# Performance work log

Hardware: AMD Instinct MI355X
Metric: run time of the kernel (lower is better)

## Reference

```python
import jax, jax.numpy as jnp
import numpy as np

EPS_SCALE = 1e-4

def setup_inputs() -> dict:
    key = jax.random.key(0)
    B, D, K = 4096, 64, 256
    x = jax.random.normal(key, (B, D, K), dtype=jnp.float32)
    return {"x": x}

def reference(x):
    # x: [B, D, K]  (batch, cluster_dim, num_clusters) -- training path
    B, D, K = x.shape
    mu = jnp.mean(x, axis=0, keepdims=True)              # [1, D, K]
    xc = jnp.transpose(x - mu, (2, 1, 0))                # [K, D, B]
    cov = jnp.einsum('kdb,keb->kde', xc, xc) / (B - 1)   # [K, D, D]
    eps = EPS_SCALE * jnp.eye(D, dtype=x.dtype)
    L = jnp.linalg.cholesky(cov + eps)                   # [K, D, D]
    Z = jax.scipy.linalg.solve_triangular(L, xc, lower=True)  # [K, D, B]
    return jnp.transpose(Z, (2, 1, 0))                   # [B, D, K]
```

## Files before the change

### kernel.cpp

```cpp
#include <hip/hip_runtime.h>
#include <math.h>

#define Bn 4096
#define Dn 64
#define Kn 256
#define DKn 16384
#define SLAB ((size_t)262144)

typedef __attribute__((ext_vector_type(8))) short bf16x8;
typedef __attribute__((ext_vector_type(4))) float f32x4;
typedef unsigned short u16;
typedef unsigned int u32;

__device__ __forceinline__ float bf2f(u16 u) {
  return __uint_as_float(((u32)u) << 16);
}
__device__ __forceinline__ u16 f2bf(float f) {
  u32 x = __float_as_uint(f);
  u32 r = x + 0x7fffu + ((x >> 16) & 1u);
  return (u16)(r >> 16);
}

__global__ __launch_bounds__(256) void k1_transpose(
    const float* __restrict__ x, u16* __restrict__ xh) {
  __shared__ float tf[64][65];
  const int b0 = blockIdx.x * 8;
  const int k0 = blockIdx.y * 64;
  const int t = threadIdx.x;
  const int kq = t & 15, dsub = t >> 4;
  const int dq = t & 7, kr = t >> 3;

  for (int bb = 0; bb < 8; ++bb) {
    const int b = b0 + bb;
#pragma unroll
    for (int i = 0; i < 4; ++i) {
      const int d = dsub + 16 * i;
      const float4 v = *(const float4*)&x[(size_t)b * DKn + (size_t)d * Kn + k0 + 4 * kq];
      tf[4 * kq + 0][d] = v.x;
      tf[4 * kq + 1][d] = v.y;
      tf[4 * kq + 2][d] = v.z;
      tf[4 * kq + 3][d] = v.w;
    }
    __syncthreads();
#pragma unroll
    for (int it = 0; it < 2; ++it) {
      const int k = kr + 32 * it;
      u32 pk[4];
#pragma unroll
      for (int j = 0; j < 4; ++j) {
        const float f0 = tf[k][8 * dq + 2 * j];
        const float f1 = tf[k][8 * dq + 2 * j + 1];
        pk[j] = (u32)f2bf(f0) | ((u32)f2bf(f1) << 16);
      }
      *(uint4*)&xh[(size_t)(k0 + k) * SLAB + (size_t)b * 64 + 8 * dq] =
          make_uint4(pk[0], pk[1], pk[2], pk[3]);
    }
    __syncthreads();
  }
}

__global__ __launch_bounds__(256) void k2_cov(
    const u16* __restrict__ xh, float* __restrict__ covp, float* __restrict__ Sp) {
  __shared__ __align__(16) u16 tile[64][136];
  __shared__ float sred[64][33];
  const int part = blockIdx.x;
  const int k = blockIdx.y;
  const int t = threadIdx.x;
  const int w = t >> 6, l = t & 63;
  const int r16 = l & 15, g = l >> 4;
  const int q = t >> 3, c = t & 7;
  const u16* pk = xh + (size_t)k * SLAB;

  f32x4 hh[10];
#pragma unroll
  for (int p = 0; p < 10; ++p) hh[p] = (f32x4){0.f, 0.f, 0.f, 0.f};
  float dsums[8];
#pragma unroll
  for (int jj = 0; jj < 8; ++jj) dsums[jj] = 0.f;

  for (int sub = 0; sub < 8; ++sub) {
    const int bbase = part * 1024 + sub * 128;
    __syncthreads();
    uint4 pv[4];
#pragma unroll
    for (int i = 0; i < 4; ++i)
      pv[i] = *(const uint4*)&pk[(size_t)(bbase + 4 * q + i) * 64 + c * 8];
    const u16* e0 = (const u16*)&pv[0];
    const u16* e1 = (const u16*)&pv[1];
    const u16* e2 = (const u16*)&pv[2];
    const u16* e3 = (const u16*)&pv[3];
#pragma unroll
    for (int jj = 0; jj < 8; ++jj) {
      const int d = 8 * c + jj;
      const int s4 = 4 * ((d >> 2) & 7);
      const u16 v0 = e0[jj], v1 = e1[jj], v2 = e2[jj], v3 = e3[jj];
      dsums[jj] += (bf2f(v0) + bf2f(v1)) + (bf2f(v2) + bf2f(v3));
      const int col0 = (2 * q) ^ s4;
      uint2 st;
      st.x = (u32)v0 | ((u32)v1 << 16);
      st.y = (u32)v2 | ((u32)v3 << 16);
      *(uint2*)&tile[d][2 * col0] = st;
    }
    __syncthreads();
    bf16x8 fr[4];
#pragma unroll
    for (int m = 0; m < 4; ++m) {
      const int d = 16 * m + r16;
      const int s4 = 4 * ((d >> 2) & 7);
      const int colb = (16 * w + 4 * g) ^ s4;
      fr[m] = *(const bf16x8*)&tile[d][2 * colb];
    }
#pragma unroll
    for (int m = 0; m < 4; ++m)
#pragma unroll
      for (int n = m; n < 4; ++n) {
        const int p = (m * (7 - m)) / 2 + n;
        hh[p] = __builtin_amdgcn_mfma_f32_16x16x32_bf16(fr[m], fr[n], hh[p], 0, 0, 0);
      }
  }
  float* cp = covp + ((size_t)k * 16 + part * 4 + w) * 2560;
#pragma unroll
  for (int p = 0; p < 10; ++p)
#pragma unroll
    for (int r = 0; r < 4; ++r)
      cp[p * 256 + (g * 4 + r) * 16 + r16] = hh[p][r];
#pragma unroll
  for (int jj = 0; jj < 8; ++jj) sred[8 * c + jj][q] = dsums[jj];
  __syncthreads();
  if (t < 64) {
    float s = 0.f;
#pragma unroll
    for (int q2 = 0; q2 < 32; ++q2) s += sred[t][q2];
    Sp[((size_t)k * 4 + part) * 64 + t] = s;
  }
}

__global__ __launch_bounds__(256) void k3_chol(
    const float* __restrict__ covp, const float* __restrict__ Sp,
    u16* __restrict__ wt, u16* __restrict__ vout) {
  __shared__ float a[64][65];
  __shared__ float mus[64];
  __shared__ float colv[64];
  __shared__ float diag;
  const int k = blockIdx.x;
  const int tid = threadIdx.x;
  if (tid < 64) {
    float s = 0.f;
#pragma unroll
    for (int q = 0; q < 4; ++q) s += Sp[((size_t)k * 4 + q) * 64 + tid];
    mus[tid] = s * (1.f / 4096.f);
  }
  __syncthreads();
  const float* cp = covp + (size_t)k * 16 * 2560;
  for (int idx = tid; idx < 4096; idx += 256) {
    const int i = idx >> 6, j = idx & 63;
    const int i16 = i >> 4, j16 = j >> 4, r = i & 15, c = j & 15;
    int p, off;
    if (i16 <= j16) { p = (i16 * (7 - i16)) / 2 + j16; off = r * 16 + c; }
    else            { p = (j16 * (7 - j16)) / 2 + i16; off = c * 16 + r; }
    float s = 0.f;
#pragma unroll
    for (int q = 0; q < 16; ++q) s += cp[q * 2560 + p * 256 + off];
    float cv = (s - 4096.f * mus[i] * mus[j]) * (1.f / 4095.f);
    if (i == j) cv += 1e-4f;
    a[i][j] = cv;
  }
  __syncthreads();
  for (int j = 0; j < 64; ++j) {
    if (tid == j) diag = sqrtf(a[j][j]);
    __syncthreads();
    const float ljj = diag;
    float lij = 0.f;
    if (tid == j) a[j][j] = ljj;
    if (tid < 64 && tid > j) {
      lij = a[tid][j] / ljj;
      a[tid][j] = lij;
      colv[tid] = lij;
    }
    __syncthreads();
    if (tid < 64 && tid > j)
      for (int e = j + 1; e <= tid; ++e) a[tid][e] -= lij * colv[e];
    __syncthreads();
  }
  float wv[64];
  if (tid < 64) {
#pragma unroll
    for (int i = 0; i < 64; ++i) {
      float s2 = (i == tid) ? 1.f : 0.f;
#pragma unroll
      for (int j = 0; j < i; ++j) s2 -= a[i][j] * wv[j];
      wv[i] = (i >= tid) ? s2 / a[i][i] : 0.f;
    }
  }
  __syncthreads();
  if (tid < 64) {
#pragma unroll
    for (int i = 0; i < 64; ++i) a[i][tid] = wv[i];
  }
  __syncthreads();
  if (tid < 64) {
    float v = 0.f;
#pragma unroll
    for (int e = 0; e < 64; ++e) v += a[tid][e] * mus[e];
    vout[(size_t)k * 64 + tid] = f2bf(v);
  }
#pragma unroll
  for (int it = 0; it < 8; ++it) {
    const int idx = it * 256 + tid;
    const int dd = idx >> 5, ep = idx & 31;
    const u32 pk2 = (u32)f2bf(a[dd][2 * ep]) | ((u32)f2bf(a[dd][2 * ep + 1]) << 16);
    *(u32*)&wt[(size_t)k * 4096 + 2 * idx] = pk2;
  }
}

union __align__(16) SMemU {
  u16 xstage[2][8][16][64];
  u32 zls[16 * 642 + 40];
};

__global__ __launch_bounds__(256) void k45_solve(
    const u16* __restrict__ xh, const u16* __restrict__ wt,
    const u16* __restrict__ vin, float* __restrict__ out) {
  __shared__ SMemU sm;
  __shared__ __align__(16) u16 vsh[32][72];
  const int b0 = blockIdx.x * 16;
  const int kc0 = blockIdx.y * 32;
  const int t = threadIdx.x;
  const int w = t >> 6, l = t & 63;
  const int r16 = l & 15, g = l >> 4;
  const int d0 = 16 * w + 4 * g;

  *(uint4*)&vsh[t >> 3][8 * (t & 7)] = *(const uint4*)&vin[(size_t)kc0 * 64 + t * 8];

  uint4 sv[4];
#pragma unroll
  for (int i = 0; i < 4; ++i) {
    const int idx = i * 256 + t;
    const int kk = idx >> 7, b = (idx >> 3) & 15, dc = idx & 7;
    sv[i] = *(const uint4*)&xh[(size_t)(kc0 + kk) * SLAB + (size_t)(b0 + b) * 64 + dc * 8];
  }
#pragma unroll
  for (int i = 0; i < 4; ++i) {
    const int idx = i * 256 + t;
    const int kk = idx >> 7, b = (idx >> 3) & 15, dc = idx & 7;
    *(uint4*)&sm.xstage[0][kk][b][(dc ^ (b & 7)) * 8] = sv[i];
  }

  bf16x8 af0[4], af1[4];
#pragma unroll
  for (int p = 0; p < 4; ++p) {
    const u16* wk = wt + (size_t)(kc0 + p) * 4096 + (16 * w + r16) * 64 + 8 * g;
    af0[p] = *(const bf16x8*)(wk);
    af1[p] = *(const bf16x8*)(wk + 32);
  }
  __syncthreads();

  u32 zr[64];

#pragma unroll
  for (int rnd = 0; rnd < 4; ++rnd) {
    if (rnd < 3) {
#pragma unroll
      for (int i = 0; i < 4; ++i) {
        const int idx = i * 256 + t;
        const int kk = idx >> 7, b = (idx >> 3) & 15, dc = idx & 7;
        sv[i] = *(const uint4*)&xh[(size_t)(kc0 + (rnd + 1) * 8 + kk) * SLAB +
                                   (size_t)(b0 + b) * 64 + dc * 8];
      }
    }
#pragma unroll
    for (int kk = 0; kk < 8; ++kk) {
      const int kidx = rnd * 8 + kk;
      const bf16x8 a0 = af0[kidx & 3];
      const bf16x8 a1 = af1[kidx & 3];
      if (kidx + 4 < 32) {
        const u16* wk = wt + (size_t)(kc0 + kidx + 4) * 4096 + (16 * w + r16) * 64 + 8 * g;
        af0[kidx & 3] = *(const bf16x8*)(wk);
        af1[kidx & 3] = *(const bf16x8*)(wk + 32);
      }
      const bf16x8 bf0 = *(const bf16x8*)&sm.xstage[rnd & 1][kk][r16][(g ^ (r16 & 7)) * 8];
      const bf16x8 bf1 = *(const bf16x8*)&sm.xstage[rnd & 1][kk][r16][((4 + g) ^ (r16 & 7)) * 8];
      f32x4 acc = (f32x4){0.f, 0.f, 0.f, 0.f};
      acc = __builtin_amdgcn_mfma_f32_16x16x32_bf16(a0, bf0, acc, 0, 0, 0);
      acc = __builtin_amdgcn_mfma_f32_16x16x32_bf16(a1, bf1, acc, 0, 0, 0);
      const uint2 vv = *(const uint2*)&vsh[kidx][d0];
      const float s0 = acc[0] - __uint_as_float(vv.x << 16);
      const float s1 = acc[1] - __uint_as_float(vv.x & 0xffff0000u);
      const float s2 = acc[2] - __uint_as_float(vv.y << 16);
      const float s3 = acc[3] - __uint_as_float(vv.y & 0xffff0000u);
      u32 plo, phi;
      asm("v_cvt_pk_bf16_f32 %0, %1, %2" : "=v"(plo) : "v"(s0), "v"(s1));
      asm("v_cvt_pk_bf16_f32 %0, %1, %2" : "=v"(phi) : "v"(s2), "v"(s3));
      zr[2 * kidx] = plo;
      zr[2 * kidx + 1] = phi;
    }
    if (rnd < 3) {
#pragma unroll
      for (int i = 0; i < 4; ++i) {
        const int idx = i * 256 + t;
        const int kk = idx >> 7, b = (idx >> 3) & 15, dc = idx & 7;
        *(uint4*)&sm.xstage[(rnd + 1) & 1][kk][b][(dc ^ (b & 7)) * 8] = sv[i];
      }
      __syncthreads();
    }
  }
  __syncthreads();

#pragma unroll
  for (int h = 0; h < 2; ++h) {
    u32 W[4][8];
#pragma unroll
    for (int r = 0; r < 4; ++r)
#pragma unroll
      for (int q2 = 0; q2 < 8; ++q2) {
        const int k2 = 16 * h + 2 * q2;
        const u32 za = zr[2 * k2 + (r >> 1)];
        const u32 zb2 = zr[2 * (k2 + 1) + (r >> 1)];
        W[r][q2] = (r & 1) ? ((za >> 16) | (zb2 & 0xffff0000u))
                           : ((za & 0xffffu) | (zb2 << 16));
      }
#pragma unroll
    for (int r = 0; r < 4; ++r) {
      u32* cp = &sm.zls[r16 * 642 + (d0 + r) * 10];
      *(uint2*)&cp[0] = make_uint2(W[r][0], W[r][1]);
      *(uint2*)&cp[2] = make_uint2(W[r][2], W[r][3]);
      *(uint2*)&cp[4] = make_uint2(W[r][4], W[r][5]);
      *(uint2*)&cp[6] = make_uint2(W[r][6], W[r][7]);
    }
    __syncthreads();
#pragma unroll
    for (int it = 0; it < 16; ++it) {
      const int c = w * 256 + it * 16 + (l >> 2);
      const int kc = l & 3;
      const int b = c >> 6, d = c & 63;
      const uint2 zw = *(const uint2*)&sm.zls[b * 642 + d * 10 + 2 * kc];
      float4 ov;
      ov.x = __uint_as_float(zw.x << 16);
      ov.y = __uint_as_float(zw.x & 0xffff0000u);
      ov.z = __uint_as_float(zw.y << 16);
      ov.w = __uint_as_float(zw.y & 0xffff0000u);
      *(float4*)&out[(size_t)(b0 + b) * DKn + (size_t)d * Kn + kc0 + 16 * h + 4 * kc] = ov;
    }
    __syncthreads();
  }
}

extern "C" void kernel_launch(void* const* d_in, const int* in_sizes, int n_in,
                              void* d_out, int out_size, void* d_ws, size_t ws_size,
                              hipStream_t stream) {
  (void)in_sizes; (void)n_in; (void)out_size;
  const float* x = (const float*)d_in[0];
  float* out = (float*)d_out;
  char* ws = (char*)d_ws;
  const size_t XH_B = 134217728;
  const size_t CP_B = 41943040;
  const size_t SP_B = 262144;
  const size_t WT_B = 2097152;
  const size_t V_B  = 32768;
  if (ws_size < XH_B + CP_B + SP_B + WT_B + V_B) return;
  u16* xh = (u16*)ws;
  float* covp = (float*)(ws + XH_B);
  float* Sp = (float*)(ws + XH_B + CP_B);
  u16* wtb = (u16*)(ws + XH_B + CP_B + SP_B);
  u16* vb  = (u16*)(ws + XH_B + CP_B + SP_B + WT_B);

  k1_transpose<<<dim3(512, 4), 256, 0, stream>>>(x, xh);
  k2_cov<<<dim3(4, 256), 256, 0, stream>>>(xh, covp, Sp);
  k3_chol<<<dim3(256), 256, 0, stream>>>(covp, Sp, wtb, vb);
  k45_solve<<<dim3(256, 8), 256, 0, stream>>>(xh, wtb, vb, out);
}
```

Measured before the change: 361.6 us.

## Double-buffer LDS in transpose and covariance kernels; single-wave Cholesky without barriers

The transpose and covariance kernels now double-buffer their shared-memory tiles. The next slab's global loads are issued before the current tile is consumed, and each iteration needs only one barrier instead of two. The Cholesky kernel runs the factorisation, inversion and mean projection in a single 64-lane wavefront, using LDS waitcnt fences instead of block-wide __syncthreads. This costs more LDS and registers in exchange for load overlap, and relies on wavefront-synchronous execution being correct.

New measurement: 357.5 us. Within noise of the previous version (-1.2%).

```diff
diff --git a/kernel.cpp b/kernel.cpp
--- a/kernel.cpp
+++ b/kernel.cpp
@@ -20,49 +20,77 @@
   u32 r = x + 0x7fffu + ((x >> 16) & 1u);
   return (u16)(r >> 16);
 }
+__device__ __forceinline__ void wave_lds_fence() {
+  asm volatile("s_waitcnt lgkmcnt(0)" ::: "memory");
+  __builtin_amdgcn_sched_barrier(0);
+}
 
 __global__ __launch_bounds__(256) void k1_transpose(
     const float* __restrict__ x, u16* __restrict__ xh) {
-  __shared__ float tf[64][65];
+  __shared__ float tf[2][64][65];
   const int b0 = blockIdx.x * 8;
   const int k0 = blockIdx.y * 64;
   const int t = threadIdx.x;
   const int kq = t & 15, dsub = t >> 4;
   const int dq = t & 7, kr = t >> 3;
 
+  float4 rv[4];
+#pragma unroll
+  for (int i = 0; i < 4; ++i)
+    rv[i] = *(const float4*)&x[(size_t)b0 * DKn + (size_t)(dsub + 16 * i) * Kn + k0 + 4 * kq];
+#pragma unroll
+  for (int i = 0; i < 4; ++i) {
+    const int d = dsub + 16 * i;
+    tf[0][4 * kq + 0][d] = rv[i].x;
+    tf[0][4 * kq + 1][d] = rv[i].y;
+    tf[0][4 * kq + 2][d] = rv[i].z;
+    tf[0][4 * kq + 3][d] = rv[i].w;
+  }
+  __syncthreads();
+
   for (int bb = 0; bb < 8; ++bb) {
-    const int b = b0 + bb;
-#pragma unroll
-    for (int i = 0; i < 4; ++i) {
-      const int d = dsub + 16 * i;
-      const float4 v = *(const float4*)&x[(size_t)b * DKn + (size_t)d * Kn + k0 + 4 * kq];
-      tf[4 * kq + 0][d] = v.x;
-      tf[4 * kq + 1][d] = v.y;
-      tf[4 * kq + 2][d] = v.z;
-      tf[4 * kq + 3][d] = v.w;
-    }
-    __syncthreads();
+    const int cur = bb & 1;
+    if (bb < 7) {
+#pragma unroll
+      for (int i = 0; i < 4; ++i)
+        rv[i] = *(const float4*)&x[(size_t)(b0 + bb + 1) * DKn +
+                                   (size_t)(dsub + 16 * i) * Kn + k0 + 4 * kq];
+    }
 #pragma unroll
     for (int it = 0; it < 2; ++it) {
       const int k = kr + 32 * it;
       u32 pk[4];
 #pragma unroll
       for (int j = 0; j < 4; ++j) {
-        const float f0 = tf[k][8 * dq + 2 * j];
-        const float f1 = tf[k][8 * dq + 2 * j + 1];
+        const float f0 = tf[cur][k][8 * dq + 2 * j];
+        const float f1 = tf[cur][k][8 * dq + 2 * j + 1];
         pk[j] = (u32)f2bf(f0) | ((u32)f2bf(f1) << 16);
       }
-      *(uint4*)&xh[(size_t)(k0 + k) * SLAB + (size_t)b * 64 + 8 * dq] =
+      *(uint4*)&xh[(size_t)(k0 + k) * SLAB + (size_t)(b0 + bb) * 64 + 8 * dq] =
           make_uint4(pk[0], pk[1], pk[2], pk[3]);
     }
-    __syncthreads();
-  }
-}
+    if (bb < 7) {
+#pragma unroll
+      for (int i = 0; i < 4; ++i) {
+        const int d = dsub + 16 * i;
+        tf[cur ^ 1][4 * kq + 0][d] = rv[i].x;
+        tf[cur ^ 1][4 * kq + 1][d] = rv[i].y;
+        tf[cur ^ 1][4 * kq + 2][d] = rv[i].z;
+        tf[cur ^ 1][4 * kq + 3][d] = rv[i].w;
+      }
+      __syncthreads();
+    }
+  }
+}
+
+union __align__(16) K2SMem {
+  u16 tile[2][64][136];
+  float sred[64][33];
+};
 
 __global__ __launch_bounds__(256) void k2_cov(
     const u16* __restrict__ xh, float* __restrict__ covp, float* __restrict__ Sp) {
-  __shared__ __align__(16) u16 tile[64][136];
-  __shared__ float sred[64][33];
+  __shared__ K2SMem s2;
   const int part = blockIdx.x;
   const int k = blockIdx.y;
   const int t = threadIdx.x;
@@ -78,37 +106,45 @@
 #pragma unroll
   for (int jj = 0; jj < 8; ++jj) dsums[jj] = 0.f;
 
+  uint4 pv[4];
+#define K2_LOAD(SUB)                                                           \
+  {                                                                            \
+    const int bbase = part * 1024 + (SUB) * 128;                               \
+    _Pragma("unroll") for (int i = 0; i < 4; ++i)                              \
+        pv[i] = *(const uint4*)&pk[(size_t)(bbase + 4 * q + i) * 64 + c * 8];  \
+  }
+#define K2_STORE(BUF)                                                          \
+  {                                                                            \
+    const u16* e0 = (const u16*)&pv[0];                                        \
+    const u16* e1 = (const u16*)&pv[1];                                        \
+    const u16* e2 = (const u16*)&pv[2];                                        \
+    const u16* e3 = (const u16*)&pv[3];                                        \
+    _Pragma("unroll") for (int jj = 0; jj < 8; ++jj) {                         \
+      const int d = 8 * c + jj;                                                \
+      const int s4 = 4 * ((d >> 2) & 7);                                       \
+      const u16 v0 = e0[jj], v1 = e1[jj], v2 = e2[jj], v3 = e3[jj];            \
+      dsums[jj] += (bf2f(v0) + bf2f(v1)) + (bf2f(v2) + bf2f(v3));              \
+      const int col0 = (2 * q) ^ s4;                                           \
+      uint2 st;                                                                \
+      st.x = (u32)v0 | ((u32)v1 << 16);                                        \
+      st.y = (u32)v2 | ((u32)v3 << 16);                                        \
+      *(uint2*)&s2.tile[BUF][d][2 * col0] = st;                                \
+    }                                                                          \
+  }
+
+  K2_LOAD(0);
+  K2_STORE(0);
+  __syncthreads();
   for (int sub = 0; sub < 8; ++sub) {
-    const int bbase = part * 1024 + sub * 128;
-    __syncthreads();
-    uint4 pv[4];
-#pragma unroll
-    for (int i = 0; i < 4; ++i)
-      pv[i] = *(const uint4*)&pk[(size_t)(bbase + 4 * q + i) * 64 + c * 8];
-    const u16* e0 = (const u16*)&pv[0];
-    const u16* e1 = (const u16*)&pv[1];
-    const u16* e2 = (const u16*)&pv[2];
-    const u16* e3 = (const u16*)&pv[3];
-#pragma unroll
-    for (int jj = 0; jj < 8; ++jj) {
-      const int d = 8 * c + jj;
-      const int s4 = 4 * ((d >> 2) & 7);
-      const u16 v0 = e0[jj], v1 = e1[jj], v2 = e2[jj], v3 = e3[jj];
-      dsums[jj] += (bf2f(v0) + bf2f(v1)) + (bf2f(v2) + bf2f(v3));
-      const int col0 = (2 * q) ^ s4;
-      uint2 st;
-      st.x = (u32)v0 | ((u32)v1 << 16);
-      st.y = (u32)v2 | ((u32)v3 << 16);
-      *(uint2*)&tile[d][2 * col0] = st;
-    }
-    __syncthreads();
+    const int cur = sub & 1;
+    if (sub < 7) K2_LOAD(sub + 1);
     bf16x8 fr[4];
 #pragma unroll
     for (int m = 0; m < 4; ++m) {
       const int d = 16 * m + r16;
       const int s4 = 4 * ((d >> 2) & 7);
       const int colb = (16 * w + 4 * g) ^ s4;
-      fr[m] = *(const bf16x8*)&tile[d][2 * colb];
+      fr[m] = *(const bf16x8*)&s2.tile[cur][d][2 * colb];
     }
 #pragma unroll
     for (int m = 0; m < 4; ++m)
@@ -117,6 +153,10 @@
         const int p = (m * (7 - m)) / 2 + n;
         hh[p] = __builtin_amdgcn_mfma_f32_16x16x32_bf16(fr[m], fr[n], hh[p], 0, 0, 0);
       }
+    if (sub < 7) {
+      K2_STORE(cur ^ 1);
+      __syncthreads();
+    }
   }
   float* cp = covp + ((size_t)k * 16 + part * 4 + w) * 2560;
 #pragma unroll
@@ -124,13 +164,14 @@
 #pragma unroll
     for (int r = 0; r < 4; ++r)
       cp[p * 256 + (g * 4 + r) * 16 + r16] = hh[p][r];
-#pragma unroll
-  for (int jj = 0; jj < 8; ++jj) sred[8 * c + jj][q] = dsums[jj];
+  __syncthreads();
+#pragma unroll
+  for (int jj = 0; jj < 8; ++jj) s2.sred[8 * c + jj][q] = dsums[jj];
   __syncthreads();
   if (t < 64) {
     float s = 0.f;
 #pragma unroll
-    for (int q2 = 0; q2 < 32; ++q2) s += sred[t][q2];
+    for (int q2 = 0; q2 < 32; ++q2) s += s2.sred[t][q2];
     Sp[((size_t)k * 4 + part) * 64 + t] = s;
   }
 }
@@ -141,7 +182,6 @@
   __shared__ float a[64][65];
   __shared__ float mus[64];
   __shared__ float colv[64];
-  __shared__ float diag;
   const int k = blockIdx.x;
   const int tid = threadIdx.x;
   if (tid < 64) {
@@ -166,24 +206,25 @@
     a[i][j] = cv;
   }
   __syncthreads();
-  for (int j = 0; j < 64; ++j) {
-    if (tid == j) diag = sqrtf(a[j][j]);
-    __syncthreads();
-    const float ljj = diag;
-    float lij = 0.f;
-    if (tid == j) a[j][j] = ljj;
-    if (tid < 64 && tid > j) {
-      lij = a[tid][j] / ljj;
-      a[tid][j] = lij;
-      colv[tid] = lij;
-    }
-    __syncthreads();
-    if (tid < 64 && tid > j)
-      for (int e = j + 1; e <= tid; ++e) a[tid][e] -= lij * colv[e];
-    __syncthreads();
-  }
-  float wv[64];
+
   if (tid < 64) {
+    for (int j = 0; j < 64; ++j) {
+      wave_lds_fence();
+      const float ljj = sqrtf(a[j][j]);
+      float lij = 0.f;
+      if (tid == j) a[j][j] = ljj;
+      if (tid > j) {
+        lij = a[tid][j] / ljj;
+        a[tid][j] = lij;
+        colv[tid] = lij;
+      }
+      wave_lds_fence();
+      if (tid > j) {
+        for (int e = j + 1; e <= tid; ++e) a[tid][e] -= lij * colv[e];
+      }
+    }
+    wave_lds_fence();
+    float wv[64];
 #pragma unroll
     for (int i = 0; i < 64; ++i) {
       float s2 = (i == tid) ? 1.f : 0.f;
@@ -191,19 +232,16 @@
       for (int j = 0; j < i; ++j) s2 -= a[i][j] * wv[j];
       wv[i] = (i >= tid) ? s2 / a[i][i] : 0.f;
     }
-  }
-  __syncthreads();
-  if (tid < 64) {
+    wave_lds_fence();
 #pragma unroll
     for (int i = 0; i < 64; ++i) a[i][tid] = wv[i];
-  }
-  __syncthreads();
-  if (tid < 64) {
+    wave_lds_fence();
     float v = 0.f;
 #pragma unroll
     for (int e = 0; e < 64; ++e) v += a[tid][e] * mus[e];
     vout[(size_t)k * 64 + tid] = f2bf(v);
   }
+  __syncthreads();
 #pragma unroll
   for (int it = 0; it < 8; ++it) {
     const int idx = it * 256 + tid;
```
